# Kernel tuning notes

Measured on AMD Instinct MI355X. Metric: run time of the kernel, lower is better.

Reference implementation:

```python
import jax, jax.numpy as jnp
import numpy as np

NEG_INF = float('-inf')


def setup_inputs() -> dict:
    key = jax.random.key(0)
    ks = jax.random.split(key, 5)
    Sq, Sk, H, D, B = 4096, 4096, 8, 128, 4
    q = jax.random.normal(ks[0], (Sq, H, D), jnp.float32)
    k_local = jax.random.normal(ks[1], (Sk, H, D), jnp.float32)
    v_local = jax.random.normal(ks[2], (Sk, H, D), jnp.float32)
    k_remote = jax.random.normal(ks[3], (Sk, H, D), jnp.float32)
    v_remote = jax.random.normal(ks[4], (Sk, H, D), jnp.float32)
    # 4 ragged range pairs: equal blocks of 1024 q-tokens <-> 1024 kv-tokens
    blk = Sq // B
    starts = jnp.arange(B, dtype=jnp.int32) * blk
    ranges = jnp.stack([starts, starts + blk], axis=1)  # [B, 2]
    return dict(
        q=q, k_local=k_local, v_local=v_local,
        k_remote=k_remote, v_remote=v_remote,
        q_ranges_local=ranges, kv_ranges_local=ranges,
        is_causal_local=jnp.ones((B,), bool),
        q_ranges_remote=ranges, kv_ranges_remote=ranges,
        is_causal_remote=jnp.zeros((B,), bool),
    )


def _range_mask(Sq, Sk, q_ranges, kv_ranges, is_causal):
    # Build [Sq, Sk] attend-mask from ragged (q,kv) range pairs.
    qpos = jnp.arange(Sq)[None, :, None]   # [1, Sq, 1]
    kpos = jnp.arange(Sk)[None, None, :]   # [1, 1, Sk]
    qs = q_ranges[:, 0][:, None, None]; qe = q_ranges[:, 1][:, None, None]
    ks = kv_ranges[:, 0][:, None, None]; ke = kv_ranges[:, 1][:, None, None]
    in_q = (qpos >= qs) & (qpos < qe)
    in_k = (kpos >= ks) & (kpos < ke)
    # bottom-right-aligned causal within each range pair
    shift = (ke - ks) - (qe - qs)
    caus = (kpos - ks) <= (qpos - qs) + shift
    m = in_q & in_k & (caus | ~is_causal[:, None, None])  # [B, Sq, Sk]
    return jnp.any(m, axis=0)  # [Sq, Sk]


def _flex_attn(q, k, v, q_ranges, kv_ranges, is_causal):
    # q: [Sq, H, D]; k, v: [Sk, H, D] -> out [Sq, H, D], lse [H, Sq]
    Sq, H, D = q.shape
    Sk = k.shape[0]
    mask = _range_mask(Sq, Sk, q_ranges, kv_ranges, is_causal)  # [Sq, Sk]
    scale = 1.0 / np.sqrt(D).astype(np.float32)
    scores = jnp.einsum('qhd,khd->hqk', q, k) * scale
    scores = jnp.where(mask[None], scores, NEG_INF)
    mx = jnp.max(scores, axis=-1)                      # [H, Sq]
    mx_safe = jnp.where(jnp.isneginf(mx), 0.0, mx)
    e = jnp.where(mask[None], jnp.exp(scores - mx_safe[..., None]), 0.0)
    s = jnp.sum(e, axis=-1)                            # [H, Sq]
    lse = jnp.where(s > 0, mx_safe + jnp.log(jnp.where(s > 0, s, 1.0)), NEG_INF)
    p = e / jnp.where(s > 0, s, 1.0)[..., None]
    out = jnp.einsum('hqk,khd->qhd', p, v)
    return out, lse


def _safe_subtract(a, b):
    both_ninf = (a == b) & jnp.isneginf(a)
    return jnp.where(both_ninf, NEG_INF, a - b)


def _correct_lse(lse1, lse2):
    mn = jnp.minimum(lse1, lse2).astype(jnp.float32)
    mx = jnp.maximum(lse1, lse2).astype(jnp.float32)
    return (mx + jax.nn.softplus(_safe_subtract(mn, mx))).astype(lse1.dtype)


def _correct_out(o1, lse1, o2, lse2, lse):
    # lse*: [H, Sq] -> weights [Sq, H, 1]
    w1 = jnp.exp(_safe_subtract(lse1, lse)).T[..., None].astype(jnp.float32)
    w2 = jnp.exp(_safe_subtract(lse2, lse)).T[..., None].astype(jnp.float32)
    return (w1 * o1 + w2 * o2).astype(o1.dtype)


def _result_correction(out_list, lse_list, overlap_degree):
    # Faithful to the original loop structure (stage 1 merged twice).
    curr_lse = _correct_lse(lse_list[0], lse_list[1])
    curr_out = _correct_out(out_list[0], lse_list[0], out_list[1], lse_list[1], curr_lse)
    for i in range(overlap_degree):
        orig_lse, orig_out = curr_lse, curr_out
        curr_lse = _correct_lse(orig_lse, lse_list[i + 1])
        curr_out = _correct_out(orig_out, orig_lse, out_list[i + 1], lse_list[i + 1], curr_lse)
    return curr_out, curr_lse


def reference(q, k_local, v_local, k_remote, v_remote,
              q_ranges_local, kv_ranges_local, is_causal_local,
              q_ranges_remote, kv_ranges_remote, is_causal_remote):
    o0, l0 = _flex_attn(q, k_local, v_local, q_ranges_local, kv_ranges_local, is_causal_local)
    o1, l1 = _flex_attn(q, k_remote, v_remote, q_ranges_remote, kv_ranges_remote, is_causal_remote)
    out, lse = _result_correction([o0, o1], [l0, l1], overlap_degree=1)
    return out, lse
```

## Files before the change

kernel.cpp:

```cpp
#include <hip/hip_runtime.h>
#include <math.h>
#include <limits.h>


constexpr int NH = 8;
constexpr int DH = 128;
#define NEG_INF (-INFINITY)

typedef __bf16 bf16x8 __attribute__((ext_vector_type(8)));
typedef float  f32x4  __attribute__((ext_vector_type(4)));
typedef float  f32x16 __attribute__((ext_vector_type(16)));

__device__ __forceinline__ unsigned short f2bf_rne(float x) {
  union { float f; unsigned u; } v; v.f = x;
  unsigned r = v.u + 0x7FFFu + ((v.u >> 16) & 1u);
  return (unsigned short)(r >> 16);
}
__device__ __forceinline__ unsigned pk2(float lo, float hi) {
  return (unsigned)f2bf_rne(lo) | ((unsigned)f2bf_rne(hi) << 16);
}
__device__ __forceinline__ unsigned cvtpk_bf16(float lo, float hi) {
  unsigned r;
  asm("v_cvt_pk_bf16_f32 %0, %1, %2" : "=v"(r) : "v"(lo), "v"(hi));
  return r;
}
__device__ __forceinline__ void gl2lds16(const void* g, void* l) {
  __builtin_amdgcn_global_load_lds(
      (const __attribute__((address_space(1))) unsigned int*)g,
      (__attribute__((address_space(3))) unsigned int*)l, 16, 0, 0);
}
#define MFMA32 __builtin_amdgcn_mfma_f32_32x32x16_bf16

__global__ void prep_kernel(const float* __restrict__ kl, const float* __restrict__ kr,
                            const float* __restrict__ vl, const float* __restrict__ vr,
                            unsigned short* __restrict__ Kb,
                            unsigned short* __restrict__ Vt, int Sk) {
  __shared__ unsigned short T[64 * 132];
  const int nk = Sk >> 2;
  const int npan = Sk >> 6;
  const int t = threadIdx.x;
  int bid = blockIdx.x;

  if (bid < 2 * nk) {
    const int src = bid >= nk;
    const int x = src ? bid - nk : bid;
    const float* in = src ? kr : kl;
    unsigned short* o = Kb + (size_t)src * NH * Sk * DH;
    const size_t base = (size_t)x * 4096;
    #pragma unroll
    for (int rdx = 0; rdx < 4; ++rdx) {
      const size_t L = base + rdx * 1024 + (size_t)t * 4;
      float4 f = *(const float4*)(in + L);
      const int kv  = (int)(L >> 10);
      const int rem = (int)(L & 1023);
      const int h = rem >> 7, d = rem & 127;
      const int pe = (((d >> 3) ^ (kv & 15)) << 3) + (d & 7);
      uint2 w = make_uint2(pk2(f.x, f.y), pk2(f.z, f.w));
      *(uint2*)&o[((size_t)h * Sk + kv) * DH + pe] = w;
    }
  } else {
    bid -= 2 * nk;
    const int nv = npan * NH;
    const int src = bid >= nv;
    if (src) bid -= nv;
    const int h = bid / npan;
    const int x = bid % npan;
    const float* in = src ? vr : vl;
    const float vscl = src ? 2.0f : 1.0f;
    const int kv0 = x * 64;
    unsigned short* panel =
        Vt + (((size_t)src * NH + h) * npan + x) * (DH * 64);
    {
      const int off = (t & 31) * 4;
      const int kvr_ = t >> 5;
      #pragma unroll
      for (int rdx = 0; rdx < 8; ++rdx) {
        const int kv = rdx * 8 + kvr_;
        float4 f = *(const float4*)(in + ((size_t)(kv0 + kv) * NH + h) * DH + off);
        *(uint2*)&T[kv * 132 + off] =
            make_uint2(pk2(f.x * vscl, f.y * vscl), pk2(f.z * vscl, f.w * vscl));
      }
    }
    __syncthreads();
    #pragma unroll
    for (int rdx = 0; rdx < 4; ++rdx) {
      const int G = rdx * 256 + t;
      const int r = G >> 4, sp = G & 15;
      const int s = sp ^ ((r & 7) << 1);
      const int d = 2 * r + (s & 1);
      const int g = s >> 1;
      unsigned short v[8];
      #pragma unroll
      for (int j = 0; j < 8; ++j) v[j] = T[(g * 8 + j) * 132 + d];
      *(uint4*)&panel[(size_t)G * 8] = *(uint4*)v;
    }
  }
}

struct TS { int src, b, kv0, qs, qe, ks, ke, causal, shift, kendb; };

__global__ __launch_bounds__(256, 2)
void fa_kernel(const float* __restrict__ qp,
               const unsigned short* __restrict__ Kb,
               const unsigned short* __restrict__ Vt,
               const int* __restrict__ qrl, const int* __restrict__ kvrl,
               const int* __restrict__ czl,
               const int* __restrict__ qrr, const int* __restrict__ kvrr,
               const int* __restrict__ czr,
               float* __restrict__ outp, float* __restrict__ lsep,
               unsigned short* __restrict__ pO, float* __restrict__ pL,
               int Sq, int Sk, int B, int nsplit, int direct)
{
  __shared__ __align__(16) unsigned short Klds[2][64 * DH];
  __shared__ __align__(16) unsigned short Vlds[2][64 * DH];
  __shared__ float Lsc[4][32];

  const int tid = threadIdx.x, wave = tid >> 6, lane = tid & 63;
  const int dl = lane & 31, hi = lane >> 5;
  const int bid = blockIdx.x;
  const int h   = bid & 7;
  const int nqt = Sq >> 7;
  const int tt  = bid >> 3;
  int qtile = tt % nqt;
  const int split = tt / nqt;
  if (split & 1) qtile = nqt - 1 - qtile;
  const int q0 = qtile * 128;
  const int qw = q0 + wave * 32;
  const int qg = qw + dl;

  const float kscale = 0.12751743f;

  bf16x8 qfB[8];
  {
    const float* gq = qp + ((size_t)qg * NH + h) * DH + hi * 8;
    #pragma unroll
    for (int dc = 0; dc < 8; ++dc) {
      float4 a = *(const float4*)(gq + dc * 16);
      float4 b = *(const float4*)(gq + dc * 16 + 4);
      uint4 t = { pk2(a.x * kscale, a.y * kscale), pk2(a.z * kscale, a.w * kscale),
                  pk2(b.x * kscale, b.y * kscale), pk2(b.z * kscale, b.w * kscale) };
      qfB[dc] = __builtin_bit_cast(bf16x8, t);
    }
  }

  f32x16 accO[4];
  #pragma unroll
  for (int i = 0; i < 4; ++i) accO[i] = (f32x16)(0.0f);
  float lacc = 0.0f;

  auto nextTile = [&](TS& t) -> bool {
    t.kv0 += nsplit * 64;
    while (t.kv0 >= t.kendb) {
      ++t.b;
      if (t.b >= B) {
        t.b = -1; ++t.src;
        if (t.src >= 2) return false;
        t.kendb = INT_MIN; t.kv0 = 0;
        continue;
      }
      const int* qr  = t.src ? qrr : qrl;
      const int* kvr = t.src ? kvrr : kvrl;
      const int* cz  = t.src ? czr : czl;
      t.qs = qr[2*t.b]; t.qe = qr[2*t.b+1];
      t.ks = kvr[2*t.b]; t.ke = kvr[2*t.b+1];
      if (t.qe <= q0 || t.qs >= q0 + 128 || t.ks >= t.ke) {
        t.kendb = INT_MIN; t.kv0 = 0; continue;
      }
      t.causal = cz[t.b] != 0;
      t.shift = (t.ke - t.ks) - (t.qe - t.qs);
      const int qmaxb = min(q0 + 127, t.qe - 1);
      t.kendb = t.causal ? min(t.ke, t.ks + (qmaxb - t.qs) + t.shift + 1) : t.ke;
      t.kv0 = ((t.ks >> 6) << 6) + split * 64;
    }
    return true;
  };

  auto stageTile = [&](const TS& t, unsigned short* lkb, unsigned short* lvb) {
    const unsigned short* kbh = Kb + ((size_t)t.src * NH + h) * (size_t)Sk * DH;
    const char* gk = (const char*)(kbh + (size_t)t.kv0 * DH) + wave * 4096 + lane * 16;
    char* lk = (char*)lkb + wave * 4096 + lane * 16;
    #pragma unroll
    for (int i = 0; i < 4; ++i) gl2lds16(gk + i * 1024, lk + i * 1024);
    const unsigned short* vth = Vt + ((size_t)t.src * NH + h) * ((size_t)(Sk >> 6) * DH * 64);
    const char* gv = (const char*)(vth + (size_t)(t.kv0 >> 6) * (DH * 64)) + wave * 4096 + lane * 16;
    char* lv = (char*)lvb + wave * 4096 + lane * 16;
    #pragma unroll
    for (int i = 0; i < 4; ++i) gl2lds16(gv + i * 1024, lv + i * 1024);
  };

  auto computeTile = [&](const TS& t, const unsigned short* kb,
                         const unsigned short* vb) {
    int wkend = INT_MIN;
    {
      const int wqs = max(qw, t.qs), wqe = min(qw + 32, t.qe);
      if (wqs < wqe) {
        const int wqmax = min(qw + 31, t.qe - 1);
        wkend = t.causal
              ? min(t.ke, t.ks + (wqmax - t.qs) + t.shift + 1)
              : t.ke;
      }
    }
    if (t.kv0 >= wkend) return;
    const int kv0 = t.kv0, ks = t.ks, ke = t.ke;
    const int qs = t.qs, qe = t.qe, causal = t.causal, shift = t.shift;

    f32x16 S0 = (f32x16)(0.0f), S1 = (f32x16)(0.0f);
    __builtin_amdgcn_s_setprio(1);
    #pragma unroll
    for (int dc = 0; dc < 8; ++dc) {
      const int ph = ((dc * 2 + hi) ^ (dl & 15)) << 3;
      bf16x8 k0 = *(const bf16x8*)&kb[dl * DH + ph];
      bf16x8 k1 = *(const bf16x8*)&kb[(32 + dl) * DH + ph];
      S0 = MFMA32(k0, qfB[dc], S0, 0, 0, 0);
      S1 = MFMA32(k1, qfB[dc], S1, 0, 0, 0);
    }
    __builtin_amdgcn_s_setprio(0);

    const bool interior = (kv0 >= ks) && (kv0 + 64 <= ke) &&
                          (qw >= qs) && (qw + 32 <= qe) &&
                          (!causal || (kv0 + 63 - ks) <= (qw - qs) + shift);
    if (!interior) {
      const int qok = (qg >= qs) && (qg < qe);
      const int lo = ks - kv0;
      int up = ke - kv0 - 1;
      if (causal) up = min(up, (qg - qs) + shift + (ks - kv0));
      #pragma unroll
      for (int r = 0; r < 16; ++r) {
        const int kt = (r & 3) + 8 * (r >> 2) + 4 * hi;
        const int ok0 = qok && (kt >= lo) && (kt <= up);
        const int ok1 = qok && (kt + 32 >= lo) && (kt + 32 <= up);
        S0[r] = ok0 ? S0[r] : NEG_INF;
        S1[r] = ok1 ? S1[r] : NEG_INF;
      }
    }

    float p0[16], p1[16];
    #pragma unroll
    for (int r = 0; r < 16; ++r) {
      p0[r] = __builtin_amdgcn_exp2f(S0[r]);
      p1[r] = __builtin_amdgcn_exp2f(S1[r]);
    }
    {
      float t0 = 0.f, t1 = 0.f, t2 = 0.f, t3 = 0.f;
      #pragma unroll
      for (int r = 0; r < 4; ++r) {
        t0 += p0[r];      t1 += p0[r + 4];
        t2 += p0[r + 8];  t3 += p0[r + 12];
        t0 += p1[r];      t1 += p1[r + 4];
        t2 += p1[r + 8];  t3 += p1[r + 12];
      }
      const float ts = (t0 + t1) + (t2 + t3);
      lacc += t.src ? 2.0f * ts : ts;
    }

    __builtin_amdgcn_s_setprio(1);
    const int vrow = (dl >> 1) * 128;
    #define PVKC(pp, kc)                                                        \
    {                                                                           \
      const unsigned a0 = cvtpk_bf16(pp[((kc)&1)*8+0], pp[((kc)&1)*8+1]);       \
      const unsigned a1 = cvtpk_bf16(pp[((kc)&1)*8+2], pp[((kc)&1)*8+3]);       \
      const unsigned b0 = cvtpk_bf16(pp[((kc)&1)*8+4], pp[((kc)&1)*8+5]);       \
      const unsigned b1 = cvtpk_bf16(pp[((kc)&1)*8+6], pp[((kc)&1)*8+7]);       \
      auto s0 = __builtin_amdgcn_permlane32_swap((int)a0, (int)b0, false, false);\
      auto s1 = __builtin_amdgcn_permlane32_swap((int)a1, (int)b1, false, false);\
      uint4 pw = { (unsigned)s0[0], (unsigned)s1[0],                            \
                   (unsigned)s0[1], (unsigned)s1[1] };                          \
      const bf16x8 pa = __builtin_bit_cast(bf16x8, pw);                         \
      const int sp = ((((kc)*2+hi) << 1) | (dl & 1)) ^ (((dl >> 1) & 7) << 1);  \
      const int vbase = vrow + sp * 8;                                          \
      _Pragma("unroll")                                                         \
      for (int dt = 0; dt < 4; ++dt) {                                          \
        bf16x8 vf = *(const bf16x8*)&vb[dt * 2048 + vbase];                     \
        accO[dt] = MFMA32(pa, vf, accO[dt], 0, 0, 0);                           \
      }                                                                         \
    }
    PVKC(p0, 0) PVKC(p0, 1) PVKC(p1, 2) PVKC(p1, 3)
    #undef PVKC
    __builtin_amdgcn_s_setprio(0);
  };

  TS cur; cur.src = 0; cur.b = -1; cur.kv0 = 0; cur.kendb = INT_MIN;
  cur.qs = 0; cur.qe = 0; cur.ks = 0; cur.ke = 0; cur.causal = 0; cur.shift = 0;
  bool hc = nextTile(cur);
  TS nx = cur;
  bool hn = hc ? nextTile(nx) : false;
  if (hc) stageTile(cur, &Klds[0][0], &Vlds[0][0]);
  __syncthreads();

  while (hc) {
    if (hn) stageTile(nx, &Klds[1][0], &Vlds[1][0]);
    computeTile(cur, &Klds[0][0], &Vlds[0][0]);
    __syncthreads();
    cur = nx; hc = hn;
    if (hc) hn = nextTile(nx);
    if (!hc) break;
    if (hn) stageTile(nx, &Klds[0][0], &Vlds[0][0]);
    computeTile(cur, &Klds[1][0], &Vlds[1][0]);
    __syncthreads();
    cur = nx; hc = hn;
    if (hc) hn = nextTile(nx);
  }

  const float tot = lacc + __shfl_xor(lacc, 32);
  if (lane < 32) Lsc[wave][lane] = tot;
  __syncthreads();

  if (direct) {
    if (lane < 32)
      lsep[(size_t)h * Sq + qg] =
          tot > 0.f ? 0.6931471805599453f * __builtin_amdgcn_logf(tot) : NEG_INF;
    #pragma unroll
    for (int r = 0; r < 16; ++r) {
      const int qrow = (r & 3) + 8 * (r >> 2) + 4 * hi;
      const float sum = Lsc[wave][qrow];
      const float rcp = sum > 0.f ? 1.0f / sum : 0.0f;
      float* op = outp + ((size_t)(qw + qrow) * NH + h) * DH + dl;
      #pragma unroll
      for (int dt = 0; dt < 4; ++dt)
        op[dt * 32] = accO[dt][r] * rcp;
    }
  } else {
    if (lane < 32) pL[((size_t)split * NH + h) * Sq + qg] = tot;
    #pragma unroll
    for (int r = 0; r < 16; ++r) {
      const int qrow = (r & 3) + 8 * (r >> 2) + 4 * hi;
      unsigned short* pr = pO + (((size_t)split * Sq + (qw + qrow)) * NH + h) * DH + dl;
      #pragma unroll
      for (int dt = 0; dt < 4; ++dt)
        pr[dt * 32] = f2bf_rne(accO[dt][r]);
    }
  }
}

__global__ void merge_kernel(const unsigned short* __restrict__ pO,
                             const float* __restrict__ pL,
                             float* __restrict__ outp, float* __restrict__ lsep,
                             int Sq, int nsplit) {
  const int t = threadIdx.x;
  const int row = blockIdx.x * 4 + (t >> 6);
  const int dp = t & 63;
  const int q = row >> 3, h = row & 7;
  float s = 0.f, o0 = 0.f, o1 = 0.f;
  for (int sp = 0; sp < nsplit; ++sp) {
    s += pL[((size_t)sp * NH + h) * Sq + q];
    unsigned u = *(const unsigned*)&pO[(((size_t)sp * Sq + q) * NH + h) * DH + dp * 2];
    o0 += __builtin_bit_cast(float, u << 16);
    o1 += __builtin_bit_cast(float, u & 0xffff0000u);
  }
  const float rcp = s > 0.f ? 1.0f / s : 0.f;
  *(float2*)&outp[(size_t)row * DH + dp * 2] = make_float2(o0 * rcp, o1 * rcp);
  if (dp == 0)
    lsep[(size_t)h * Sq + q] =
        s > 0.f ? 0.6931471805599453f * __builtin_amdgcn_logf(s) : NEG_INF;
}

extern "C" void kernel_launch(void* const* d_in, const int* in_sizes, int n_in,
                              void* d_out, int out_size, void* d_ws, size_t ws_size,
                              hipStream_t stream) {
  const float* qp = (const float*)d_in[0];
  const float* kl = (const float*)d_in[1];
  const float* vl = (const float*)d_in[2];
  const float* kr = (const float*)d_in[3];
  const float* vr = (const float*)d_in[4];
  const int* qrl  = (const int*)d_in[5];
  const int* kvrl = (const int*)d_in[6];
  const int* czl  = (const int*)d_in[7];
  const int* qrr  = (const int*)d_in[8];
  const int* kvrr = (const int*)d_in[9];
  const int* czr  = (const int*)d_in[10];

  const int B  = in_sizes[5] / 2;
  const int Sq = in_sizes[0] / (NH * DH);
  const int Sk = in_sizes[1] / (NH * DH);
  float* outp = (float*)d_out;
  float* lsep = outp + (size_t)Sq * NH * DH;

  const size_t TEN  = (size_t)NH * Sk * DH;
  const size_t base = 4 * TEN * sizeof(unsigned short);
  unsigned short* Kb = (unsigned short*)d_ws;
  unsigned short* Vt = Kb + 2 * TEN;

  auto needO = [&](int ns) {
    return (size_t)ns * Sq * NH * DH * 2 + (size_t)ns * NH * Sq * 4;
  };
  int ns; int direct = 0;
  if      (ws_size >= base + needO(2)) ns = 2;
  else if (ws_size >= base + needO(1)) ns = 1;
  else { ns = 1; direct = 1; }
  unsigned short* pO = (unsigned short*)((char*)d_ws + base);
  float* pL = (float*)((char*)d_ws + base + (size_t)ns * Sq * NH * DH * 2);

  const int prep_blocks = 2 * (Sk / 4) + 2 * (Sk / 64) * NH;
  prep_kernel<<<dim3(prep_blocks), 256, 0, stream>>>(kl, kr, vl, vr, Kb, Vt, Sk);

  fa_kernel<<<dim3(ns * (Sq / 128) * NH), 256, 0, stream>>>(
      qp, Kb, Vt, qrl, kvrl, czl, qrr, kvrr, czr,
      outp, lsep, pO, pL, Sq, Sk, B, ns, direct);

  if (!direct)
    merge_kernel<<<dim3(Sq * NH / 4), 256, 0, stream>>>(pO, pL, outp, lsep, Sq, ns);
}
```

Before: 177.2 us.

## Fuse split-K merge into attention kernel via per-tile atomic counters

Removes the separate merge kernel. Each (head, q-tile) pair now has an atomic counter: the first of the two split blocks to finish writes its partial output and sum, and the last one reads the partner's partial, combines it with its own registers and writes the final output and LSE. This saves a kernel launch and a full round trip of one partial buffer, at the cost of a memset, atomics, fences, and a fallback path that drops ns=1 non-direct mode.

```diff
diff --git a/kernel.cpp b/kernel.cpp
--- a/kernel.cpp
+++ b/kernel.cpp
@@ -109,11 +109,13 @@
                const int* __restrict__ czr,
                float* __restrict__ outp, float* __restrict__ lsep,
                unsigned short* __restrict__ pO, float* __restrict__ pL,
+               unsigned* __restrict__ cnt,
                int Sq, int Sk, int B, int nsplit, int direct)
 {
   __shared__ __align__(16) unsigned short Klds[2][64 * DH];
   __shared__ __align__(16) unsigned short Vlds[2][64 * DH];
   __shared__ float Lsc[4][32];
+  __shared__ unsigned role;
 
   const int tid = threadIdx.x, wave = tid >> 6, lane = tid & 63;
   const int dl = lane & 31, hi = lane >> 5;
@@ -302,13 +304,14 @@
   }
 
   const float tot = lacc + __shfl_xor(lacc, 32);
-  if (lane < 32) Lsc[wave][lane] = tot;
-  __syncthreads();
 
   if (direct) {
-    if (lane < 32)
+    if (lane < 32) {
+      Lsc[wave][lane] = tot;
       lsep[(size_t)h * Sq + qg] =
           tot > 0.f ? 0.6931471805599453f * __builtin_amdgcn_logf(tot) : NEG_INF;
+    }
+    __syncthreads();
     #pragma unroll
     for (int r = 0; r < 16; ++r) {
       const int qrow = (r & 3) + 8 * (r >> 2) + 4 * hi;
@@ -319,7 +322,17 @@
       for (int dt = 0; dt < 4; ++dt)
         op[dt * 32] = accO[dt][r] * rcp;
     }
-  } else {
+    return;
+  }
+
+  const int cidx = h * nqt + (q0 >> 7);
+  const int ps = split ^ 1;
+
+  if (tid == 0)
+    role = (atomicAdd(&cnt[cidx], 0u) != 0) ? 1u : 0u;
+  __syncthreads();
+
+  if (role == 0) {
     if (lane < 32) pL[((size_t)split * NH + h) * Sq + qg] = tot;
     #pragma unroll
     for (int r = 0; r < 16; ++r) {
@@ -329,29 +342,38 @@
       for (int dt = 0; dt < 4; ++dt)
         pr[dt * 32] = f2bf_rne(accO[dt][r]);
     }
-  }
-}
-
-__global__ void merge_kernel(const unsigned short* __restrict__ pO,
-                             const float* __restrict__ pL,
-                             float* __restrict__ outp, float* __restrict__ lsep,
-                             int Sq, int nsplit) {
-  const int t = threadIdx.x;
-  const int row = blockIdx.x * 4 + (t >> 6);
-  const int dp = t & 63;
-  const int q = row >> 3, h = row & 7;
-  float s = 0.f, o0 = 0.f, o1 = 0.f;
-  for (int sp = 0; sp < nsplit; ++sp) {
-    s += pL[((size_t)sp * NH + h) * Sq + q];
-    unsigned u = *(const unsigned*)&pO[(((size_t)sp * Sq + q) * NH + h) * DH + dp * 2];
-    o0 += __builtin_bit_cast(float, u << 16);
-    o1 += __builtin_bit_cast(float, u & 0xffff0000u);
-  }
-  const float rcp = s > 0.f ? 1.0f / s : 0.f;
-  *(float2*)&outp[(size_t)row * DH + dp * 2] = make_float2(o0 * rcp, o1 * rcp);
-  if (dp == 0)
-    lsep[(size_t)h * Sq + q] =
-        s > 0.f ? 0.6931471805599453f * __builtin_amdgcn_logf(s) : NEG_INF;
+    __syncthreads();
+    if (tid == 0) {
+      __threadfence();
+      const unsigned old = atomicAdd(&cnt[cidx], 1u);
+      role = (old == 1) ? 1u : 2u;
+    }
+    __syncthreads();
+    if (role == 2) return;
+  }
+
+  __threadfence();
+  if (lane < 32) {
+    const float s2 = tot + pL[((size_t)ps * NH + h) * Sq + qg];
+    Lsc[wave][lane] = s2;
+    lsep[(size_t)h * Sq + qg] =
+        s2 > 0.f ? 0.6931471805599453f * __builtin_amdgcn_logf(s2) : NEG_INF;
+  }
+  __syncthreads();
+  #pragma unroll
+  for (int r = 0; r < 16; ++r) {
+    const int qrow = (r & 3) + 8 * (r >> 2) + 4 * hi;
+    const float sum = Lsc[wave][qrow];
+    const float rcp = sum > 0.f ? 1.0f / sum : 0.0f;
+    const int q = qw + qrow;
+    const unsigned short* pr2 = pO + (((size_t)ps * Sq + q) * NH + h) * DH + dl;
+    float* op = outp + ((size_t)q * NH + h) * DH + dl;
+    #pragma unroll
+    for (int dt = 0; dt < 4; ++dt) {
+      const unsigned u = (unsigned)pr2[dt * 32] << 16;
+      op[dt * 32] = (accO[dt][r] + __builtin_bit_cast(float, u)) * rcp;
+    }
+  }
 }
 
 extern "C" void kernel_launch(void* const* d_in, const int* in_sizes, int n_in,
@@ -380,23 +402,27 @@
   unsigned short* Kb = (unsigned short*)d_ws;
   unsigned short* Vt = Kb + 2 * TEN;
 
-  auto needO = [&](int ns) {
-    return (size_t)ns * Sq * NH * DH * 2 + (size_t)ns * NH * Sq * 4;
+  auto needO = [&](int ns_) {
+    return (size_t)ns_ * Sq * NH * DH * 2 + (size_t)ns_ * NH * Sq * 4;
   };
-  int ns; int direct = 0;
-  if      (ws_size >= base + needO(2)) ns = 2;
-  else if (ws_size >= base + needO(1)) ns = 1;
+  const int nqt = Sq / 128;
+  const size_t cntB = (size_t)nqt * NH * sizeof(unsigned);
+
+  int ns, direct;
+  if (ws_size >= base + needO(2) + cntB) { ns = 2; direct = 0; }
   else { ns = 1; direct = 1; }
+
   unsigned short* pO = (unsigned short*)((char*)d_ws + base);
   float* pL = (float*)((char*)d_ws + base + (size_t)ns * Sq * NH * DH * 2);
+  unsigned* cnt = (unsigned*)((char*)d_ws + base + needO(ns));
+
+  if (!direct)
+    hipMemsetAsync(cnt, 0, cntB, stream);
 
   const int prep_blocks = 2 * (Sk / 4) + 2 * (Sk / 64) * NH;
   prep_kernel<<<dim3(prep_blocks), 256, 0, stream>>>(kl, kr, vl, vr, Kb, Vt, Sk);
 
-  fa_kernel<<<dim3(ns * (Sq / 128) * NH), 256, 0, stream>>>(
+  fa_kernel<<<dim3(ns * nqt * NH), 256, 0, stream>>>(
       qp, Kb, Vt, qrl, kvrl, czl, qrr, kvrr, czr,
-      outp, lsep, pO, pL, Sq, Sk, B, ns, direct);
-
-  if (!direct)
-    merge_kernel<<<dim3(Sq * NH / 4), 256, 0, stream>>>(pO, pL, outp, lsep, Sq, ns);
-}
+      outp, lsep, pO, pL, cnt, Sq, Sk, B, ns, direct);
+}
```

New measurement: 216.2 us. 22.0% more time.

## Read V fragments directly from global memory instead of staging through LDS

Applied to the files above, without the earlier changes.

Drops the double-buffered V tile from shared memory: the PV MFMA fragments are now loaded straight from the pre-transposed V panels in global memory (L2/L1), and the LDS bank-conflict swizzle in the V layout and its read indexing is removed. Halving LDS use allows launch bounds to rise to 3 blocks per CU for more occupancy. The cost is global-load latency sitting directly in the PV loop with no async prefetch, plus more register pressure under the higher occupancy target.

```diff
diff --git a/kernel.cpp b/kernel.cpp
--- a/kernel.cpp
+++ b/kernel.cpp
@@ -86,9 +86,8 @@
     for (int rdx = 0; rdx < 4; ++rdx) {
       const int G = rdx * 256 + t;
       const int r = G >> 4, sp = G & 15;
-      const int s = sp ^ ((r & 7) << 1);
-      const int d = 2 * r + (s & 1);
-      const int g = s >> 1;
+      const int d = 2 * r + (sp & 1);
+      const int g = sp >> 1;
       unsigned short v[8];
       #pragma unroll
       for (int j = 0; j < 8; ++j) v[j] = T[(g * 8 + j) * 132 + d];
@@ -99,7 +98,7 @@
 
 struct TS { int src, b, kv0, qs, qe, ks, ke, causal, shift, kendb; };
 
-__global__ __launch_bounds__(256, 2)
+__global__ __launch_bounds__(256, 3)
 void fa_kernel(const float* __restrict__ qp,
                const unsigned short* __restrict__ Kb,
                const unsigned short* __restrict__ Vt,
@@ -112,7 +111,6 @@
                int Sq, int Sk, int B, int nsplit, int direct)
 {
   __shared__ __align__(16) unsigned short Klds[2][64 * DH];
-  __shared__ __align__(16) unsigned short Vlds[2][64 * DH];
   __shared__ float Lsc[4][32];
 
   const int tid = threadIdx.x, wave = tid >> 6, lane = tid & 63;
@@ -175,21 +173,15 @@
     return true;
   };
 
-  auto stageTile = [&](const TS& t, unsigned short* lkb, unsigned short* lvb) {
+  auto stageTile = [&](const TS& t, unsigned short* lkb) {
     const unsigned short* kbh = Kb + ((size_t)t.src * NH + h) * (size_t)Sk * DH;
     const char* gk = (const char*)(kbh + (size_t)t.kv0 * DH) + wave * 4096 + lane * 16;
     char* lk = (char*)lkb + wave * 4096 + lane * 16;
     #pragma unroll
     for (int i = 0; i < 4; ++i) gl2lds16(gk + i * 1024, lk + i * 1024);
-    const unsigned short* vth = Vt + ((size_t)t.src * NH + h) * ((size_t)(Sk >> 6) * DH * 64);
-    const char* gv = (const char*)(vth + (size_t)(t.kv0 >> 6) * (DH * 64)) + wave * 4096 + lane * 16;
-    char* lv = (char*)lvb + wave * 4096 + lane * 16;
-    #pragma unroll
-    for (int i = 0; i < 4; ++i) gl2lds16(gv + i * 1024, lv + i * 1024);
   };
 
-  auto computeTile = [&](const TS& t, const unsigned short* kb,
-                         const unsigned short* vb) {
+  auto computeTile = [&](const TS& t, const unsigned short* kb) {
     int wkend = INT_MIN;
     {
       const int wqs = max(qw, t.qs), wqe = min(qw + 32, t.qe);
@@ -203,6 +195,9 @@
     if (t.kv0 >= wkend) return;
     const int kv0 = t.kv0, ks = t.ks, ke = t.ke;
     const int qs = t.qs, qe = t.qe, causal = t.causal, shift = t.shift;
+    const unsigned short* vgp =
+        Vt + ((size_t)t.src * NH + h) * ((size_t)(Sk >> 6) * DH * 64)
+           + (size_t)(kv0 >> 6) * (DH * 64);
 
     f32x16 S0 = (f32x16)(0.0f), S1 = (f32x16)(0.0f);
     __builtin_amdgcn_s_setprio(1);
@@ -266,11 +261,11 @@
       uint4 pw = { (unsigned)s0[0], (unsigned)s1[0],                            \
                    (unsigned)s0[1], (unsigned)s1[1] };                          \
       const bf16x8 pa = __builtin_bit_cast(bf16x8, pw);                         \
-      const int sp = ((((kc)*2+hi) << 1) | (dl & 1)) ^ (((dl >> 1) & 7) << 1);  \
+      const int sp = (((kc) * 2 + hi) << 1) | (dl & 1);        \
       const int vbase = vrow + sp * 8;                                          \
       _Pragma("unroll")                                                         \
       for (int dt = 0; dt < 4; ++dt) {                                          \
-        bf16x8 vf = *(const bf16x8*)&vb[dt * 2048 + vbase];                     \
+        bf16x8 vf = *(const bf16x8*)&vgp[dt * 2048 + vbase];                    \
         accO[dt] = MFMA32(pa, vf, accO[dt], 0, 0, 0);                           \
       }                                                                         \
     }
@@ -284,18 +279,18 @@
   bool hc = nextTile(cur);
   TS nx = cur;
   bool hn = hc ? nextTile(nx) : false;
-  if (hc) stageTile(cur, &Klds[0][0], &Vlds[0][0]);
+  if (hc) stageTile(cur, &Klds[0][0]);
   __syncthreads();
 
   while (hc) {
-    if (hn) stageTile(nx, &Klds[1][0], &Vlds[1][0]);
-    computeTile(cur, &Klds[0][0], &Vlds[0][0]);
+    if (hn) stageTile(nx, &Klds[1][0]);
+    computeTile(cur, &Klds[0][0]);
     __syncthreads();
     cur = nx; hc = hn;
     if (hc) hn = nextTile(nx);
     if (!hc) break;
-    if (hn) stageTile(nx, &Klds[0][0], &Vlds[0][0]);
-    computeTile(cur, &Klds[1][0], &Vlds[1][0]);
+    if (hn) stageTile(nx, &Klds[0][0]);
+    computeTile(cur, &Klds[1][0]);
     __syncthreads();
     cur = nx; hc = hn;
     if (hc) hn = nextTile(nx);
@@ -380,8 +375,8 @@
   unsigned short* Kb = (unsigned short*)d_ws;
   unsigned short* Vt = Kb + 2 * TEN;
 
-  auto needO = [&](int ns) {
-    return (size_t)ns * Sq * NH * DH * 2 + (size_t)ns * NH * Sq * 4;
+  auto needO = [&](int ns_) {
+    return (size_t)ns_ * Sq * NH * DH * 2 + (size_t)ns_ * NH * Sq * 4;
   };
   int ns; int direct = 0;
   if      (ws_size >= base + needO(2)) ns = 2;
```

New measurement: 203.5 us. 14.9% more time.

## Single-buffer V in LDS, raise occupancy to three blocks, use three KV splits

Applied to the files above, without the earlier changes.

V now has a single LDS buffer instead of two. V for the current tile is loaded while QK runs, and the next K is prefetched during PV. This frees LDS so launch bounds can ask for three blocks per CU. The KV split count rises to three when the workspace allows it, and q-tiles are rotated per split to balance the causal work. The cost is an extra barrier per tile, exposed V load latency, and tighter register limits that could cause spills.

```diff
diff --git a/kernel.cpp b/kernel.cpp
--- a/kernel.cpp
+++ b/kernel.cpp
@@ -99,7 +99,7 @@
 
 struct TS { int src, b, kv0, qs, qe, ks, ke, causal, shift, kendb; };
 
-__global__ __launch_bounds__(256, 2)
+__global__ __launch_bounds__(256, 3)
 void fa_kernel(const float* __restrict__ qp,
                const unsigned short* __restrict__ Kb,
                const unsigned short* __restrict__ Vt,
@@ -112,7 +112,7 @@
                int Sq, int Sk, int B, int nsplit, int direct)
 {
   __shared__ __align__(16) unsigned short Klds[2][64 * DH];
-  __shared__ __align__(16) unsigned short Vlds[2][64 * DH];
+  __shared__ __align__(16) unsigned short Vlds[64 * DH];
   __shared__ float Lsc[4][32];
 
   const int tid = threadIdx.x, wave = tid >> 6, lane = tid & 63;
@@ -121,9 +121,8 @@
   const int h   = bid & 7;
   const int nqt = Sq >> 7;
   const int tt  = bid >> 3;
-  int qtile = tt % nqt;
   const int split = tt / nqt;
-  if (split & 1) qtile = nqt - 1 - qtile;
+  const int qtile = (tt % nqt + (split * nqt) / nsplit) % nqt;
   const int q0 = qtile * 128;
   const int qw = q0 + wave * 32;
   const int qg = qw + dl;
@@ -175,21 +174,24 @@
     return true;
   };
 
-  auto stageTile = [&](const TS& t, unsigned short* lkb, unsigned short* lvb) {
+  auto stageK = [&](const TS& t, unsigned short* lkb) {
     const unsigned short* kbh = Kb + ((size_t)t.src * NH + h) * (size_t)Sk * DH;
     const char* gk = (const char*)(kbh + (size_t)t.kv0 * DH) + wave * 4096 + lane * 16;
     char* lk = (char*)lkb + wave * 4096 + lane * 16;
     #pragma unroll
     for (int i = 0; i < 4; ++i) gl2lds16(gk + i * 1024, lk + i * 1024);
+  };
+
+  auto stageV = [&](const TS& t) {
     const unsigned short* vth = Vt + ((size_t)t.src * NH + h) * ((size_t)(Sk >> 6) * DH * 64);
     const char* gv = (const char*)(vth + (size_t)(t.kv0 >> 6) * (DH * 64)) + wave * 4096 + lane * 16;
-    char* lv = (char*)lvb + wave * 4096 + lane * 16;
+    char* lv = (char*)Vlds + wave * 4096 + lane * 16;
     #pragma unroll
     for (int i = 0; i < 4; ++i) gl2lds16(gv + i * 1024, lv + i * 1024);
   };
 
-  auto computeTile = [&](const TS& t, const unsigned short* kb,
-                         const unsigned short* vb) {
+  auto computeQK = [&](const TS& t, const unsigned short* kb,
+                       float (&p0)[16], float (&p1)[16]) -> bool {
     int wkend = INT_MIN;
     {
       const int wqs = max(qw, t.qs), wqe = min(qw + 32, t.qe);
@@ -200,7 +202,7 @@
               : t.ke;
       }
     }
-    if (t.kv0 >= wkend) return;
+    if (t.kv0 >= wkend) return false;
     const int kv0 = t.kv0, ks = t.ks, ke = t.ke;
     const int qs = t.qs, qe = t.qe, causal = t.causal, shift = t.shift;
 
@@ -234,7 +236,6 @@
       }
     }
 
-    float p0[16], p1[16];
     #pragma unroll
     for (int r = 0; r < 16; ++r) {
       p0[r] = __builtin_amdgcn_exp2f(S0[r]);
@@ -252,7 +253,10 @@
       const float ts = (t0 + t1) + (t2 + t3);
       lacc += t.src ? 2.0f * ts : ts;
     }
-
+    return true;
+  };
+
+  auto computePV = [&](float (&p0)[16], float (&p1)[16]) {
     __builtin_amdgcn_s_setprio(1);
     const int vrow = (dl >> 1) * 128;
     #define PVKC(pp, kc)                                                        \
@@ -270,7 +274,7 @@
       const int vbase = vrow + sp * 8;                                          \
       _Pragma("unroll")                                                         \
       for (int dt = 0; dt < 4; ++dt) {                                          \
-        bf16x8 vf = *(const bf16x8*)&vb[dt * 2048 + vbase];                     \
+        bf16x8 vf = *(const bf16x8*)&Vlds[dt * 2048 + vbase];                   \
         accO[dt] = MFMA32(pa, vf, accO[dt], 0, 0, 0);                           \
       }                                                                         \
     }
@@ -284,19 +288,31 @@
   bool hc = nextTile(cur);
   TS nx = cur;
   bool hn = hc ? nextTile(nx) : false;
-  if (hc) stageTile(cur, &Klds[0][0], &Vlds[0][0]);
+  if (hc) stageK(cur, &Klds[0][0]);
   __syncthreads();
 
   while (hc) {
-    if (hn) stageTile(nx, &Klds[1][0], &Vlds[1][0]);
-    computeTile(cur, &Klds[0][0], &Vlds[0][0]);
-    __syncthreads();
+    {
+      stageV(cur);
+      float p0[16], p1[16];
+      const bool live = computeQK(cur, &Klds[0][0], p0, p1);
+      __syncthreads();
+      if (hn) stageK(nx, &Klds[1][0]);
+      if (live) computePV(p0, p1);
+      __syncthreads();
+    }
     cur = nx; hc = hn;
     if (hc) hn = nextTile(nx);
     if (!hc) break;
-    if (hn) stageTile(nx, &Klds[0][0], &Vlds[0][0]);
-    computeTile(cur, &Klds[1][0], &Vlds[1][0]);
-    __syncthreads();
+    {
+      stageV(cur);
+      float p0[16], p1[16];
+      const bool live = computeQK(cur, &Klds[1][0], p0, p1);
+      __syncthreads();
+      if (hn) stageK(nx, &Klds[0][0]);
+      if (live) computePV(p0, p1);
+      __syncthreads();
+    }
     cur = nx; hc = hn;
     if (hc) hn = nextTile(nx);
   }
@@ -380,11 +396,12 @@
   unsigned short* Kb = (unsigned short*)d_ws;
   unsigned short* Vt = Kb + 2 * TEN;
 
-  auto needO = [&](int ns) {
-    return (size_t)ns * Sq * NH * DH * 2 + (size_t)ns * NH * Sq * 4;
+  auto needO = [&](int ns_) {
+    return (size_t)ns_ * Sq * NH * DH * 2 + (size_t)ns_ * NH * Sq * 4;
   };
   int ns; int direct = 0;
-  if      (ws_size >= base + needO(2)) ns = 2;
+  if      (ws_size >= base + needO(3)) ns = 3;
+  else if (ws_size >= base + needO(2)) ns = 2;
   else if (ws_size >= base + needO(1)) ns = 1;
   else { ns = 1; direct = 1; }
   unsigned short* pO = (unsigned short*)((char*)d_ws + base);
```

Measured after the change: 232.7 us. 31.4% more time.
